# Optimization experiments

Measured on AMD Instinct MI355X. Metric: run time of the kernel, lower is better.

## Reference

```python
import jax, jax.numpy as jnp
import numpy as np

D = 512      # d_model
H = 8        # n_heads
NB = 6       # n_blocks
V = 32000    # vocab
F = 2048     # ff_size
B, L = 2, 1024
EPS = 1e-6
NEG = -1e10  # -INF used by create_causal_bias


def _ln(x, g, b):
    m = jnp.mean(x, axis=-1, keepdims=True)
    v = jnp.mean((x - m) ** 2, axis=-1, keepdims=True)
    return (x - m) * jax.lax.rsqrt(v + EPS) * g + b


def _split_heads(t):
    b, l, _ = t.shape
    return t.reshape(b, l, H, D // H).transpose(0, 2, 1, 3)  # [B,H,L,dh]


def _mha(q_in, kv_in, bias, wq, wk, wv, wo):
    # manual q@k^T / sqrt(dh) + bias -> softmax -> @v -> out proj (no bias terms)
    q = _split_heads(q_in @ wq)
    k = _split_heads(kv_in @ wk)
    v = _split_heads(kv_in @ wv)
    s = jnp.einsum('bhqd,bhkd->bhqk', q, k) / (D // H) ** 0.5 + bias
    a = jax.nn.softmax(s, axis=-1)
    o = jnp.einsum('bhqk,bhkd->bhqd', a, v)
    b_, _, l, _ = o.shape
    o = o.transpose(0, 2, 1, 3).reshape(b_, l, D)
    return o @ wo


def _pos_enc(length):
    pos = jnp.arange(length, dtype=jnp.float32)
    half = D // 2
    i = jnp.arange(half, dtype=jnp.float32)
    scaled = pos[:, None] / jnp.power(10000.0, i / half)[None]
    return jnp.concatenate([jnp.sin(scaled), jnp.cos(scaled)], axis=1)  # [L, D]


def setup_inputs() -> dict:
    key = jax.random.key(0)
    ks = jax.random.split(key, 16)
    s = 0.02
    inp = {
        'x': jax.random.randint(ks[0], (B, L), 0, V, dtype=jnp.int32),
        'ctx': jax.random.normal(ks[1], (B, L, D), jnp.float32),
        'emb': jax.random.normal(ks[2], (V, D), jnp.float32) * s,
        'wq_s': jax.random.normal(ks[3], (NB, D, D), jnp.float32) * s,
        'wk_s': jax.random.normal(ks[4], (NB, D, D), jnp.float32) * s,
        'wv_s': jax.random.normal(ks[5], (NB, D, D), jnp.float32) * s,
        'wo_s': jax.random.normal(ks[6], (NB, D, D), jnp.float32) * s,
        'wq_c': jax.random.normal(ks[7], (NB, D, D), jnp.float32) * s,
        'wk_c': jax.random.normal(ks[8], (NB, D, D), jnp.float32) * s,
        'wv_c': jax.random.normal(ks[9], (NB, D, D), jnp.float32) * s,
        'wo_c': jax.random.normal(ks[10], (NB, D, D), jnp.float32) * s,
        'w1': jax.random.normal(ks[11], (NB, D, F), jnp.float32) * s,
        'b1': jnp.zeros((NB, F), jnp.float32),
        'w2': jax.random.normal(ks[12], (NB, F, D), jnp.float32) * s,
        'b2': jnp.zeros((NB, D), jnp.float32),
        'ln1_g': jnp.ones((NB, D), jnp.float32), 'ln1_b': jnp.zeros((NB, D), jnp.float32),
        'ln2_g': jnp.ones((NB, D), jnp.float32), 'ln2_b': jnp.zeros((NB, D), jnp.float32),
        'ln3_g': jnp.ones((NB, D), jnp.float32), 'ln3_b': jnp.zeros((NB, D), jnp.float32),
        'lnf_g': jnp.ones((D,), jnp.float32), 'lnf_b': jnp.zeros((D,), jnp.float32),
    }
    return inp


def reference(x, ctx, emb, wq_s, wk_s, wv_s, wo_s, wq_c, wk_c, wv_c, wo_c,
              w1, b1, w2, b2, ln1_g, ln1_b, ln2_g, ln2_b, ln3_g, ln3_b,
              lnf_g, lnf_b):
    length = x.shape[1]
    # embedding * sqrt(D) + sinusoidal positional encoding
    h = emb[x] * jnp.sqrt(jnp.float32(D)) + _pos_enc(length)[None]
    # causal bias: upper triangle (excl. diag) filled with -INF, shape [1,1,L,L]
    causal = ((1.0 - jnp.tril(jnp.ones((length, length), jnp.float32))) * NEG)[None, None]
    zero_bias = jnp.zeros((1, 1, 1, 1), jnp.float32)  # no masking of encoder ctx
    for i in range(NB):
        y = _ln(h, ln1_g[i], ln1_b[i])
        h = h + _mha(y, y, causal, wq_s[i], wk_s[i], wv_s[i], wo_s[i])
        y = _ln(h, ln2_g[i], ln2_b[i])
        h = h + _mha(y, ctx, zero_bias, wq_c[i], wk_c[i], wv_c[i], wo_c[i])
        y = _ln(h, ln3_g[i], ln3_b[i])
        h = h + (jax.nn.relu(y @ w1[i] + b1[i]) @ w2[i] + b2[i])
    h = _ln(h, lnf_g, lnf_b)
    # emb2logits: shared embedding projection
    return jnp.einsum('bld,vd->blv', h, emb)
```

## Files before the change

### kernel.cpp

```cpp
#include <hip/hip_runtime.h>
#include <math.h>

#define Bv 2
#define Lv 1024
#define Dv 512
#define Hv 8
#define DH 64
#define Fv 2048
#define NBv 6
#define Vv 32000
#define Mv (Bv*Lv)
#define QS 1536
#define KVS 6144
#define NEGINF -1e10f

typedef __attribute__((ext_vector_type(8))) short short8;
typedef __attribute__((ext_vector_type(4))) short short4v;
typedef __attribute__((ext_vector_type(4))) float floatx4;
typedef __attribute__((address_space(1))) const void gvoid;
typedef __attribute__((address_space(3))) void svoid;

__device__ __forceinline__ short f2bf(float f) {
    union { float f; unsigned u; } v; v.f = f;
    unsigned r = v.u + 0x7fffu + ((v.u >> 16) & 1u);
    return (short)(r >> 16);
}

__global__ __launch_bounds__(256)
void embed_kernel(const int* __restrict__ xi, const float* __restrict__ emb,
                  float* __restrict__ h)
{
    const int row = blockIdx.x;
    const int l   = row & (Lv - 1);
    const int tok = xi[row];
    const int tid = threadIdx.x;
#pragma unroll
    for (int s = 0; s < 2; ++s) {
        const int d  = tid + s * 256;
        const int dd = d & 255;
        const float freq = powf(10000.f, (float)dd * (1.f / 256.f));
        const float arg  = (float)l / freq;
        const float pe   = (d < 256) ? sinf(arg) : cosf(arg);
        h[(size_t)row * Dv + d] = emb[(size_t)tok * Dv + d] * 22.62741699796952f + pe;
    }
}

__global__ __launch_bounds__(256)
void cvt_kernel(const float* __restrict__ X, short* __restrict__ Y)
{
    const int i = (blockIdx.x * 256 + threadIdx.x) * 4;
    const float4 v = *(const float4*)(X + i);
    short4v p; p.x = f2bf(v.x); p.y = f2bf(v.y); p.z = f2bf(v.z); p.w = f2bf(v.w);
    *(short4v*)(Y + i) = p;
}

__global__ __launch_bounds__(256)
void tr_cvt(const float* __restrict__ src, short* __restrict__ dst,
            int K, int N, size_t dstZ, size_t dstOff)
{
    __shared__ float t[64][65];
    const int z  = blockIdx.z;
    const int n0 = blockIdx.x * 64, k0 = blockIdx.y * 64;
    const int tid = threadIdx.x;
    const float* s = src + (size_t)z * K * N;
    short* d = dst + (size_t)z * dstZ + dstOff;

    const int kr = tid >> 2, nc = (tid & 3) * 16;
#pragma unroll
    for (int j = 0; j < 16; j += 4) {
        const float4 v = *(const float4*)(s + (size_t)(k0 + kr) * N + n0 + nc + j);
        t[kr][nc + j + 0] = v.x; t[kr][nc + j + 1] = v.y;
        t[kr][nc + j + 2] = v.z; t[kr][nc + j + 3] = v.w;
    }
    __syncthreads();
    const int nr = tid >> 2, kc = (tid & 3) * 16;
    short8 o0, o1;
#pragma unroll
    for (int j = 0; j < 8; ++j)  o0[j] = f2bf(t[kc + j][nr]);
#pragma unroll
    for (int j = 0; j < 8; ++j)  o1[j] = f2bf(t[kc + 8 + j][nr]);
    *(short8*)(d + (size_t)(n0 + nr) * K + k0 + kc)     = o0;
    *(short8*)(d + (size_t)(n0 + nr) * K + k0 + kc + 8) = o1;
}

__global__ __launch_bounds__(256)
void ln_kernel(const float* __restrict__ X, const float* __restrict__ g,
               const float* __restrict__ bta, short* __restrict__ Y)
{
    const int row = blockIdx.x, tid = threadIdx.x;
    const float* xr = X + (size_t)row * Dv;
    const float x0 = xr[tid], x1 = xr[tid + 256];
    __shared__ float red[4];

    float s = x0 + x1;
#pragma unroll
    for (int off = 32; off; off >>= 1) s += __shfl_xor(s, off);
    if ((tid & 63) == 0) red[tid >> 6] = s;
    __syncthreads();
    const float mean = (red[0] + red[1] + red[2] + red[3]) * (1.f / Dv);
    __syncthreads();

    const float d0 = x0 - mean, d1 = x1 - mean;
    float v = d0 * d0 + d1 * d1;
#pragma unroll
    for (int off = 32; off; off >>= 1) v += __shfl_xor(v, off);
    if ((tid & 63) == 0) red[tid >> 6] = v;
    __syncthreads();
    const float var  = (red[0] + red[1] + red[2] + red[3]) * (1.f / Dv);
    const float rstd = rsqrtf(var + 1e-6f);

    Y[(size_t)row * Dv + tid]       = f2bf(d0 * rstd * g[tid]       + bta[tid]);
    Y[(size_t)row * Dv + tid + 256] = f2bf(d1 * rstd * g[tid + 256] + bta[tid + 256]);
}

template <int BM, int BN, int BK, int BMODE, bool OUTBF, bool SWZ, bool DBUF>
__global__ __launch_bounds__(256)
void mgemm(const short* __restrict__ A, const float* __restrict__ B,
           void* __restrict__ Cp, int M, int N, int K,
           const float* __restrict__ bias,
           const float* __restrict__ residual, int relu)
{
    constexpr int WMT = BM / 2, MI = WMT / 16, NF = BN / 32;
    constexpr int CPR = BK / 8;
    constexpr int NBUF = (DBUF && BMODE == 2) ? 2 : 1;
    __shared__ short As[NBUF * BM * BK];
    __shared__ short Bs[NBUF * BN * BK];
    const int tid  = threadIdx.x;
    const int wave = tid >> 6, lane = tid & 63;
    const int wm = wave & 1, wn = wave >> 1;
    const int quad = lane >> 4, l16 = lane & 15;

    int m0, n0;
    if (SWZ) {
        const int wg = (blockIdx.x & 7) * 500 + (blockIdx.x >> 3);
        m0 = (wg & 15) * BM;
        n0 = (wg >> 4) * BN;
    } else {
        m0 = blockIdx.y * BM;
        n0 = blockIdx.x * BN;
    }

    floatx4 acc[MI][NF];
#pragma unroll
    for (int i = 0; i < MI; ++i)
#pragma unroll
        for (int j = 0; j < NF; ++j)
            acc[i][j] = (floatx4){0.f, 0.f, 0.f, 0.f};

    auto computeTile = [&](const short* Asb, const short* Bsb) {
#pragma unroll
        for (int kk = 0; kk < BK; kk += 32) {
            short8 af[MI];
#pragma unroll
            for (int mi = 0; mi < MI; ++mi) {
                const int r = wm * WMT + mi * 16 + l16;
                af[mi] = *(const short8*)&Asb[r * BK + ((kk + quad * 8) ^ ((r & 7) << 3))];
            }
#pragma unroll
            for (int ni = 0; ni < NF; ++ni) {
                const int n = wn * (BN / 2) + ni * 16 + l16;
                const short8 bfr = *(const short8*)&Bsb[n * BK + ((kk + quad * 8) ^ ((n & 7) << 3))];
#pragma unroll
                for (int mi = 0; mi < MI; ++mi)
                    acc[mi][ni] = __builtin_amdgcn_mfma_f32_16x16x32_bf16(af[mi], bfr, acc[mi][ni], 0, 0, 0);
            }
        }
    };

    if constexpr (DBUF && BMODE == 2) {
        const short* Bb = (const short*)B;
        auto stage = [&](int buf, int kbase) {
#pragma unroll
            for (int s = 0; s < (BM * CPR) / 256; ++s) {
                const int c = s * 256 + tid;
                const int row = c / CPR, kp = (c % CPR) * 8;
                const int kps = kp ^ ((row & 7) << 3);
                const short* gp = A + (size_t)(m0 + row) * K + kbase + kps;
                __builtin_amdgcn_global_load_lds((gvoid*)gp,
                    (svoid*)((char*)As + buf * (BM * BK * 2) + c * 16), 16, 0, 0);
            }
#pragma unroll
            for (int s = 0; s < (BN * CPR) / 256; ++s) {
                const int c = s * 256 + tid;
                const int row = c / CPR, kp = (c % CPR) * 8;
                const int kps = kp ^ ((row & 7) << 3);
                const short* gp = Bb + (size_t)(n0 + row) * K + kbase + kps;
                __builtin_amdgcn_global_load_lds((gvoid*)gp,
                    (svoid*)((char*)Bs + buf * (BN * BK * 2) + c * 16), 16, 0, 0);
            }
        };
        stage(0, 0);
        __syncthreads();
        const int NT = K / BK;
        for (int t = 0; t < NT; ++t) {
            const int cur = t & 1;
            if (t + 1 < NT) stage(cur ^ 1, (t + 1) * BK);
            computeTile(As + cur * BM * BK, Bs + cur * BN * BK);
            __syncthreads();
        }
    } else {
        for (int k0 = 0; k0 < K; k0 += BK) {
            __syncthreads();
#pragma unroll
            for (int s = 0; s < (BM * CPR) / 256; ++s) {
                const int c = s * 256 + tid;
                const int row = c / CPR, kp = (c % CPR) * 8;
                const int kps = kp ^ ((row & 7) << 3);
                const short* gp = A + (size_t)(m0 + row) * K + k0 + kps;
                __builtin_amdgcn_global_load_lds((gvoid*)gp, (svoid*)((char*)As + c * 16),
                                                 16, 0, 0);
            }
            if (BMODE == 0) {
                constexpr int QN = BN / 4;
                constexpr int KSTEP = (256 / QN) * 4;
                const int qn  = tid % QN;
                const int kq0 = (tid / QN) * 4;
#pragma unroll
                for (int p = 0; p < BK / KSTEP; ++p) {
                    const int krow = p * KSTEP + kq0;
                    const float* gp = B + (size_t)(k0 + krow) * N + n0 + qn * 4;
                    const float4 r0 = *(const float4*)(gp);
                    const float4 r1 = *(const float4*)(gp + N);
                    const float4 r2 = *(const float4*)(gp + 2 * (size_t)N);
                    const float4 r3 = *(const float4*)(gp + 3 * (size_t)N);
#pragma unroll
                    for (int e = 0; e < 4; ++e) {
                        const int n = qn * 4 + e;
                        short4v p4;
                        p4.x = f2bf(e == 0 ? r0.x : e == 1 ? r0.y : e == 2 ? r0.z : r0.w);
                        p4.y = f2bf(e == 0 ? r1.x : e == 1 ? r1.y : e == 2 ? r1.z : r1.w);
                        p4.z = f2bf(e == 0 ? r2.x : e == 1 ? r2.y : e == 2 ? r2.z : r2.w);
                        p4.w = f2bf(e == 0 ? r3.x : e == 1 ? r3.y : e == 2 ? r3.z : r3.w);
                        *(short4v*)&Bs[n * BK + (krow ^ ((n & 7) << 3))] = p4;
                    }
                }
            } else if (BMODE == 1) {
#pragma unroll
                for (int f = 0; f < (BN * (BK / 4)) / 256; ++f) {
                    const int gidx = f * 256 + tid;
                    const int n = gidx / (BK / 4), q = (gidx % (BK / 4)) * 4;
                    const float4 r = *(const float4*)(B + (size_t)(n0 + n) * K + k0 + q);
                    short4v p; p.x = f2bf(r.x); p.y = f2bf(r.y); p.z = f2bf(r.z); p.w = f2bf(r.w);
                    *(short4v*)&Bs[n * BK + (q ^ ((n & 7) << 3))] = p;
                }
            } else {
                const short* Bb = (const short*)B;
#pragma unroll
                for (int s = 0; s < (BN * CPR) / 256; ++s) {
                    const int c = s * 256 + tid;
                    const int row = c / CPR, kp = (c % CPR) * 8;
                    const int kps = kp ^ ((row & 7) << 3);
                    const short* gp = Bb + (size_t)(n0 + row) * K + k0 + kps;
                    __builtin_amdgcn_global_load_lds((gvoid*)gp, (svoid*)((char*)Bs + c * 16),
                                                     16, 0, 0);
                }
            }
            __syncthreads();
            computeTile(As, Bs);
        }
    }

#pragma unroll
    for (int mi = 0; mi < MI; ++mi)
#pragma unroll
        for (int ni = 0; ni < NF; ++ni)
#pragma unroll
            for (int r = 0; r < 4; ++r) {
                const int m = m0 + wm * WMT + mi * 16 + quad * 4 + r;
                const int n = n0 + wn * (BN / 2) + ni * 16 + l16;
                float v = acc[mi][ni][r];
                if (bias)     v += bias[n];
                if (residual) v += residual[(size_t)m * N + n];
                if (relu)     v = fmaxf(v, 0.f);
                if (OUTBF) ((short*)Cp)[(size_t)m * N + n] = f2bf(v);
                else       ((float*)Cp)[(size_t)m * N + n] = v;
            }
}

__global__ __launch_bounds__(256)
void qkv_gemm(const short* __restrict__ Aq, const short* __restrict__ Akv,
              const float* __restrict__ B0, const float* __restrict__ B1,
              const float* __restrict__ B2, short* __restrict__ QKV)
{
    constexpr int BM = 64, BN = 64, BK = 64, N = Dv, K = Dv;
    constexpr int WMT = BM / 2, MI = WMT / 16, NF = 2;
    constexpr int CPR = BK / 8;
    __shared__ short As[BM * BK];
    __shared__ short Bs[BN * BK];
    const int tid  = threadIdx.x;
    const int wave = tid >> 6, lane = tid & 63;
    const int wm = wave & 1, wn = wave >> 1;
    const int quad = lane >> 4, l16 = lane & 15;
    const int n0g = blockIdx.x * BN, m0 = blockIdx.y * BM;
    const int wsel = n0g >> 9, n0 = n0g & 511;
    const short* A = (wsel == 0) ? Aq : Akv;
    const float* B = (wsel == 0) ? B0 : (wsel == 1) ? B1 : B2;

    floatx4 acc[MI][NF];
#pragma unroll
    for (int i = 0; i < MI; ++i)
#pragma unroll
        for (int j = 0; j < NF; ++j)
            acc[i][j] = (floatx4){0.f, 0.f, 0.f, 0.f};

    for (int k0 = 0; k0 < K; k0 += BK) {
        __syncthreads();
#pragma unroll
        for (int s = 0; s < (BM * CPR) / 256; ++s) {
            const int c = s * 256 + tid;
            const int row = c / CPR, kp = (c % CPR) * 8;
            const int kps = kp ^ ((row & 7) << 3);
            const short* gp = A + (size_t)(m0 + row) * K + k0 + kps;
            __builtin_amdgcn_global_load_lds((gvoid*)gp, (svoid*)((char*)As + c * 16),
                                             16, 0, 0);
        }
        {
            constexpr int QN = BN / 4;
            const int qn  = tid % QN;
            const int krow = (tid / QN) * 4;
            const float* gp = B + (size_t)(k0 + krow) * N + n0 + qn * 4;
            const float4 r0 = *(const float4*)(gp);
            const float4 r1 = *(const float4*)(gp + N);
            const float4 r2 = *(const float4*)(gp + 2 * (size_t)N);
            const float4 r3 = *(const float4*)(gp + 3 * (size_t)N);
#pragma unroll
            for (int e = 0; e < 4; ++e) {
                const int n = qn * 4 + e;
                short4v p4;
                p4.x = f2bf(e == 0 ? r0.x : e == 1 ? r0.y : e == 2 ? r0.z : r0.w);
                p4.y = f2bf(e == 0 ? r1.x : e == 1 ? r1.y : e == 2 ? r1.z : r1.w);
                p4.z = f2bf(e == 0 ? r2.x : e == 1 ? r2.y : e == 2 ? r2.z : r2.w);
                p4.w = f2bf(e == 0 ? r3.x : e == 1 ? r3.y : e == 2 ? r3.z : r3.w);
                *(short4v*)&Bs[n * BK + (krow ^ ((n & 7) << 3))] = p4;
            }
        }
        __syncthreads();
#pragma unroll
        for (int kk = 0; kk < BK; kk += 32) {
            short8 af[MI];
#pragma unroll
            for (int mi = 0; mi < MI; ++mi) {
                const int r = wm * WMT + mi * 16 + l16;
                af[mi] = *(short8*)&As[r * BK + ((kk + quad * 8) ^ ((r & 7) << 3))];
            }
#pragma unroll
            for (int ni = 0; ni < NF; ++ni) {
                const int n = wn * 32 + ni * 16 + l16;
                const short8 bfr = *(short8*)&Bs[n * BK + ((kk + quad * 8) ^ ((n & 7) << 3))];
#pragma unroll
                for (int mi = 0; mi < MI; ++mi)
                    acc[mi][ni] = __builtin_amdgcn_mfma_f32_16x16x32_bf16(af[mi], bfr, acc[mi][ni], 0, 0, 0);
            }
        }
    }

#pragma unroll
    for (int mi = 0; mi < MI; ++mi)
#pragma unroll
        for (int ni = 0; ni < NF; ++ni)
#pragma unroll
            for (int r = 0; r < 4; ++r) {
                const int m = m0 + wm * WMT + mi * 16 + quad * 4 + r;
                const int n = n0g + wn * 32 + ni * 16 + l16;
                QKV[(size_t)m * QS + n] = f2bf(acc[mi][ni][r]);
            }
}

__global__ __launch_bounds__(256)
void attn_mfma(const short* __restrict__ Qp, int qstr,
               const short* __restrict__ Kp, const short* __restrict__ Vp, int kvstr,
               short* __restrict__ Op, int causal)
{
    constexpr int PK = 72;
    __shared__ short Ks[64 * PK];
    __shared__ short Vs[64 * PK];
    __shared__ short Ps[4][16 * PK];
    const int tid  = threadIdx.x;
    const int wave = tid >> 6, lane = tid & 63;
    const int quad = lane >> 4, l16 = lane & 15;
    const int hh = blockIdx.y, bb = blockIdx.z;
    const int q0 = blockIdx.x * 64;
    const size_t qbase  = (size_t)bb * Lv * qstr  + (size_t)hh * DH;
    const size_t kvbase = (size_t)bb * Lv * kvstr + (size_t)hh * DH;
    const size_t obase  = (size_t)bb * Lv * Dv + (size_t)hh * DH;

    short8 aq[2];
    {
        const short* qp = Qp + qbase + (size_t)(q0 + wave * 16 + l16) * qstr + quad * 8;
        aq[0] = *(const short8*)qp;
        aq[1] = *(const short8*)(qp + 32);
    }

    floatx4 o[4];
#pragma unroll
    for (int i = 0; i < 4; ++i) o[i] = (floatx4){0.f, 0.f, 0.f, 0.f};
    float mrow[4] = {-3.4e38f, -3.4e38f, -3.4e38f, -3.4e38f};
    float srow[4] = {0.f, 0.f, 0.f, 0.f};

    const int ntiles = causal ? (q0 / 64 + 1) : (Lv / 64);

    for (int t = 0; t < ntiles; ++t) {
        const int j0 = t * 64;
        __syncthreads();
#pragma unroll
        for (int s = 0; s < 2; ++s) {
            const int c = s * 256 + tid;
            const int j = c >> 3, off = (c & 7) * 8;
            const size_t grow = kvbase + (size_t)(j0 + j) * kvstr + off;
            *(short8*)&Ks[j * PK + off] = *(const short8*)(Kp + grow);
            const short8 v = *(const short8*)(Vp + grow);
            const int jx = j ^ ((c & 7) << 3);
#pragma unroll
            for (int e = 0; e < 8; ++e)
                Vs[(off + e) * PK + jx] = v[e];
        }
        __syncthreads();

        floatx4 sf[4];
#pragma unroll
        for (int nf = 0; nf < 4; ++nf) {
            const short8 bk0 = *(const short8*)&Ks[(nf * 16 + l16) * PK + quad * 8];
            const short8 bk1 = *(const short8*)&Ks[(nf * 16 + l16) * PK + 32 + quad * 8];
            floatx4 z = (floatx4){0.f, 0.f, 0.f, 0.f};
            z = __builtin_amdgcn_mfma_f32_16x16x32_bf16(aq[0], bk0, z, 0, 0, 0);
            z = __builtin_amdgcn_mfma_f32_16x16x32_bf16(aq[1], bk1, z, 0, 0, 0);
            sf[nf] = z;
        }

        const bool mask = causal && (j0 == q0);
#pragma unroll
        for (int nf = 0; nf < 4; ++nf) {
            const int jabs = j0 + nf * 16 + l16;
#pragma unroll
            for (int r = 0; r < 4; ++r) {
                float v = sf[nf][r] * 0.125f;
                if (mask && jabs > q0 + wave * 16 + quad * 4 + r) v = NEGINF;
                sf[nf][r] = v;
            }
        }

#pragma unroll
        for (int r = 0; r < 4; ++r) {
            float v = fmaxf(fmaxf(sf[0][r], sf[1][r]), fmaxf(sf[2][r], sf[3][r]));
            v = fmaxf(v, __shfl_xor(v, 1));
            v = fmaxf(v, __shfl_xor(v, 2));
            v = fmaxf(v, __shfl_xor(v, 4));
            v = fmaxf(v, __shfl_xor(v, 8));
            const float mnew = fmaxf(mrow[r], v);
            const float corr = __expf(mrow[r] - mnew);
            mrow[r] = mnew;
            srow[r] *= corr;
#pragma unroll
            for (int nf = 0; nf < 4; ++nf) o[nf][r] *= corr;
        }

#pragma unroll
        for (int nf = 0; nf < 4; ++nf) {
#pragma unroll
            for (int r = 0; r < 4; ++r) {
                const float pv = __expf(sf[nf][r] - mrow[r]);
                srow[r] += pv;
                Ps[wave][(quad * 4 + r) * PK + nf * 16 + l16] = f2bf(pv);
            }
        }
        __builtin_amdgcn_wave_barrier();

        const short8 pa0 = *(const short8*)&Ps[wave][l16 * PK + quad * 8];
        const short8 pa1 = *(const short8*)&Ps[wave][l16 * PK + 32 + quad * 8];
#pragma unroll
        for (int nf = 0; nf < 4; ++nf) {
            const int d   = nf * 16 + l16;
            const int swz = ((d >> 3) & 7) << 3;
            const short8 bv0 = *(const short8*)&Vs[d * PK + ((quad * 8) ^ swz)];
            const short8 bv1 = *(const short8*)&Vs[d * PK + ((32 + quad * 8) ^ swz)];
            o[nf] = __builtin_amdgcn_mfma_f32_16x16x32_bf16(pa0, bv0, o[nf], 0, 0, 0);
            o[nf] = __builtin_amdgcn_mfma_f32_16x16x32_bf16(pa1, bv1, o[nf], 0, 0, 0);
        }
    }

#pragma unroll
    for (int r = 0; r < 4; ++r) {
        float s = srow[r];
        s += __shfl_xor(s, 1);
        s += __shfl_xor(s, 2);
        s += __shfl_xor(s, 4);
        s += __shfl_xor(s, 8);
        srow[r] = 1.f / s;
    }
#pragma unroll
    for (int nf = 0; nf < 4; ++nf)
#pragma unroll
        for (int r = 0; r < 4; ++r) {
            const size_t addr = obase + (size_t)(q0 + wave * 16 + quad * 4 + r) * Dv
                              + nf * 16 + l16;
            Op[addr] = f2bf(o[nf][r] * srow[r]);
        }
}

extern "C" void kernel_launch(void* const* d_in, const int* in_sizes, int n_in,
                              void* d_out, int out_size, void* d_ws, size_t ws_size,
                              hipStream_t stream)
{
    const int*   x    = (const int*)  d_in[0];
    const float* ctx  = (const float*)d_in[1];
    const float* emb  = (const float*)d_in[2];
    const float* wq_s = (const float*)d_in[3];
    const float* wk_s = (const float*)d_in[4];
    const float* wv_s = (const float*)d_in[5];
    const float* wo_s = (const float*)d_in[6];
    const float* wq_c = (const float*)d_in[7];
    const float* wk_c = (const float*)d_in[8];
    const float* wv_c = (const float*)d_in[9];
    const float* wo_c = (const float*)d_in[10];
    const float* w1   = (const float*)d_in[11];
    const float* b1   = (const float*)d_in[12];
    const float* w2   = (const float*)d_in[13];
    const float* b2   = (const float*)d_in[14];
    const float* ln1g = (const float*)d_in[15];
    const float* ln1b = (const float*)d_in[16];
    const float* ln2g = (const float*)d_in[17];
    const float* ln2b = (const float*)d_in[18];
    const float* ln3g = (const float*)d_in[19];
    const float* ln3b = (const float*)d_in[20];
    const float* lnfg = (const float*)d_in[21];
    const float* lnfb = (const float*)d_in[22];
    float* out = (float*)d_out;

    char* wsb = (char*)d_ws;
    const dim3 blk(256);
    const dim3 gAttn(Lv / 64, Hv, Bv);
    const dim3 gV(16 * 250);

    if (ws_size >= (150u << 20)) {
        float* h      = (float*)(wsb);
        short* y_bf   = (short*)(wsb + (4u   << 20));
        short* ao_bf  = (short*)(wsb + (6u   << 20));
        short* ctx_bf = (short*)(wsb + (8u   << 20));
        short* qkv    = (short*)(wsb + (10u  << 20));
        short* ff_bf  = (short*)(wsb + (16u  << 20));
        short* qb     = (short*)(wsb + (24u  << 20));
        short* kvc    = (short*)(wsb + (26u  << 20));
        short* wqkv_s = (short*)(wsb + (50u  << 20));
        short* wo_s_t = (short*)(wsb + (60u  << 20));
        short* wq_c_t = (short*)(wsb + (64u  << 20));
        short* wo_c_t = (short*)(wsb + (68u  << 20));
        short* kvw    = (short*)(wsb + (72u  << 20));
        short* w1t    = (short*)(wsb + (79u  << 20));
        short* w2t    = (short*)(wsb + (92u  << 20));
        short* emb_bf = (short*)(wsb + (105u << 20));

        embed_kernel<<<Mv, blk, 0, stream>>>(x, emb, h);
        cvt_kernel<<<(Mv * Dv) / 1024, blk, 0, stream>>>(ctx, ctx_bf);
        cvt_kernel<<<(Vv * Dv) / 1024, blk, 0, stream>>>(emb, emb_bf);

        const dim3 gT55(8, 8, NBv);
        const dim3 gT5F(Fv / 64, 8, NBv);
        const dim3 gTF5(8, Fv / 64, NBv);
        tr_cvt<<<gT55, blk, 0, stream>>>(wq_s, wqkv_s, Dv, Dv, (size_t)QS * Dv, 0);
        tr_cvt<<<gT55, blk, 0, stream>>>(wk_s, wqkv_s, Dv, Dv, (size_t)QS * Dv, (size_t)Dv * Dv);
        tr_cvt<<<gT55, blk, 0, stream>>>(wv_s, wqkv_s, Dv, Dv, (size_t)QS * Dv, (size_t)2 * Dv * Dv);
        tr_cvt<<<gT55, blk, 0, stream>>>(wo_s, wo_s_t, Dv, Dv, (size_t)Dv * Dv, 0);
        tr_cvt<<<gT55, blk, 0, stream>>>(wq_c, wq_c_t, Dv, Dv, (size_t)Dv * Dv, 0);
        tr_cvt<<<gT55, blk, 0, stream>>>(wo_c, wo_c_t, Dv, Dv, (size_t)Dv * Dv, 0);
        tr_cvt<<<gT55, blk, 0, stream>>>(wk_c, kvw, Dv, Dv, (size_t)2 * Dv * Dv, 0);
        tr_cvt<<<gT55, blk, 0, stream>>>(wv_c, kvw, Dv, Dv, (size_t)2 * Dv * Dv, (size_t)Dv * Dv);
        tr_cvt<<<gT5F, blk, 0, stream>>>(w1, w1t, Dv, Fv, (size_t)Fv * Dv, 0);
        tr_cvt<<<gTF5, blk, 0, stream>>>(w2, w2t, Fv, Dv, (size_t)Dv * Fv, 0);

        {
            const dim3 g(KVS / 64, Mv / 128);
            mgemm<128, 64, 64, 2, true, false, true><<<g, blk, 0, stream>>>(
                ctx_bf, (const float*)kvw, kvc, Mv, KVS, Dv, nullptr, nullptr, 0);
        }

        const dim3 gQKV(QS / 64, Mv / 64);
        const dim3 gD(Dv / 64, Mv / 32);
        const dim3 gF1(Fv / 128, Mv / 64);

        for (int i = 0; i < NBv; ++i) {
            ln_kernel<<<Mv, blk, 0, stream>>>(h, ln1g + i * Dv, ln1b + i * Dv, y_bf);
            mgemm<64, 64, 64, 2, true, false, true><<<gQKV, blk, 0, stream>>>(
                y_bf, (const float*)(wqkv_s + (size_t)i * QS * Dv), qkv,
                Mv, QS, Dv, nullptr, nullptr, 0);
            attn_mfma<<<gAttn, blk, 0, stream>>>(qkv, QS, qkv + 512, qkv + 1024, QS, ao_bf, 1);
            mgemm<32, 64, 64, 2, false, false, true><<<gD, blk, 0, stream>>>(
                ao_bf, (const float*)(wo_s_t + (size_t)i * Dv * Dv), h,
                Mv, Dv, Dv, nullptr, h, 0);
            ln_kernel<<<Mv, blk, 0, stream>>>(h, ln2g + i * Dv, ln2b + i * Dv, y_bf);
            mgemm<32, 64, 64, 2, true, false, true><<<gD, blk, 0, stream>>>(
                y_bf, (const float*)(wq_c_t + (size_t)i * Dv * Dv), qb,
                Mv, Dv, Dv, nullptr, nullptr, 0);
            attn_mfma<<<gAttn, blk, 0, stream>>>(qb, Dv,
                kvc + (size_t)i * 1024, kvc + (size_t)i * 1024 + 512, KVS, ao_bf, 0);
            mgemm<32, 64, 64, 2, false, false, true><<<gD, blk, 0, stream>>>(
                ao_bf, (const float*)(wo_c_t + (size_t)i * Dv * Dv), h,
                Mv, Dv, Dv, nullptr, h, 0);
            ln_kernel<<<Mv, blk, 0, stream>>>(h, ln3g + i * Dv, ln3b + i * Dv, y_bf);
            mgemm<64, 128, 64, 2, true, false, true><<<gF1, blk, 0, stream>>>(
                y_bf, (const float*)(w1t + (size_t)i * Fv * Dv), ff_bf,
                Mv, Fv, Dv, b1 + (size_t)i * Fv, nullptr, 1);
            mgemm<32, 64, 64, 2, false, false, true><<<gD, blk, 0, stream>>>(
                ff_bf, (const float*)(w2t + (size_t)i * Dv * Fv), h,
                Mv, Dv, Fv, b2 + (size_t)i * Dv, h, 0);
        }

        ln_kernel<<<Mv, blk, 0, stream>>>(h, lnfg, lnfb, y_bf);
        mgemm<128, 128, 64, 2, false, true, false><<<gV, blk, 0, stream>>>(
            y_bf, (const float*)emb_bf, out, Mv, Vv, Dv, nullptr, nullptr, 0);
    } else {
        float* h      = (float*)(wsb);
        short* y_bf   = (short*)(wsb + (4u  << 20));
        short* ao_bf  = (short*)(wsb + (6u  << 20));
        short* ctx_bf = (short*)(wsb + (8u  << 20));
        short* qkv    = (short*)(wsb + (10u << 20));
        short* ff_bf  = (short*)(wsb + (10u << 20));
        short* emb_bf = (short*)(wsb + (18u << 20));
        const bool fastv = ws_size >= (52u << 20);

        const dim3 gQKV(QS / 64, Mv / 64);
        const dim3 gD(Dv / 64, Mv / 32);
        const dim3 gF(Fv / 128, Mv / 64);

        embed_kernel<<<Mv, blk, 0, stream>>>(x, emb, h);
        cvt_kernel<<<(Mv * Dv) / 1024, blk, 0, stream>>>(ctx, ctx_bf);
        if (fastv)
            cvt_kernel<<<(Vv * Dv) / 1024, blk, 0, stream>>>(emb, emb_bf);

        for (int i = 0; i < NBv; ++i) {
            const size_t wOff = (size_t)i * Dv * Dv;
            ln_kernel<<<Mv, blk, 0, stream>>>(h, ln1g + i * Dv, ln1b + i * Dv, y_bf);
            qkv_gemm<<<gQKV, blk, 0, stream>>>(y_bf, y_bf,
                                               wq_s + wOff, wk_s + wOff, wv_s + wOff, qkv);
            attn_mfma<<<gAttn, blk, 0, stream>>>(qkv, QS, qkv + 512, qkv + 1024, QS, ao_bf, 1);
            mgemm<32, 64, 64, 0, false, false, false><<<gD, blk, 0, stream>>>(
                ao_bf, wo_s + wOff, h, Mv, Dv, Dv, nullptr, h, 0);
            ln_kernel<<<Mv, blk, 0, stream>>>(h, ln2g + i * Dv, ln2b + i * Dv, y_bf);
            qkv_gemm<<<gQKV, blk, 0, stream>>>(y_bf, ctx_bf,
                                               wq_c + wOff, wk_c + wOff, wv_c + wOff, qkv);
            attn_mfma<<<gAttn, blk, 0, stream>>>(qkv, QS, qkv + 512, qkv + 1024, QS, ao_bf, 0);
            mgemm<32, 64, 64, 0, false, false, false><<<gD, blk, 0, stream>>>(
                ao_bf, wo_c + wOff, h, Mv, Dv, Dv, nullptr, h, 0);
            ln_kernel<<<Mv, blk, 0, stream>>>(h, ln3g + i * Dv, ln3b + i * Dv, y_bf);
            mgemm<64, 128, 64, 0, true, false, false><<<gF, blk, 0, stream>>>(
                y_bf, w1 + (size_t)i * Dv * Fv, ff_bf, Mv, Fv, Dv,
                b1 + (size_t)i * Fv, nullptr, 1);
            mgemm<32, 64, 64, 0, false, false, false><<<gD, blk, 0, stream>>>(
                ff_bf, w2 + (size_t)i * Fv * Dv, h, Mv, Dv, Fv,
                b2 + (size_t)i * Dv, h, 0);
        }

        ln_kernel<<<Mv, blk, 0, stream>>>(h, lnfg, lnfb, y_bf);
        if (fastv)
            mgemm<128, 128, 64, 2, false, true, false><<<gV, blk, 0, stream>>>(
                y_bf, (const float*)emb_bf, out, Mv, Vv, Dv, nullptr, nullptr, 0);
        else
            mgemm<128, 128, 64, 1, false, true, false><<<gV, blk, 0, stream>>>(
                y_bf, emb, out, Mv, Vv, Dv, nullptr, nullptr, 0);
    }
}
```

Before: 1.407 ms.

## Fuse layernorm into following GEMMs and double-buffer the vocab projection

Adds an lngemm kernel that loads a 32-row fp32 tile of h, computes layernorm statistics in-block, writes normalized bf16 rows into LDS, then runs an MFMA GEMM over the full K=512 with double-buffered B tiles. It replaces the ln_kernel plus GEMM pairs for QKV, cross-attn Q and FF1, removing the y_bf round trip and three launches per block. Each tile recomputes the layernorm for its rows, so the work is repeated across N-tiles. Smaller M-tiles also change occupancy. The final vocab GEMM is switched to double buffering.

```diff
diff --git a/kernel.cpp b/kernel.cpp
--- a/kernel.cpp
+++ b/kernel.cpp
@@ -111,6 +111,124 @@
 
     Y[(size_t)row * Dv + tid]       = f2bf(d0 * rstd * g[tid]       + bta[tid]);
     Y[(size_t)row * Dv + tid + 256] = f2bf(d1 * rstd * g[tid + 256] + bta[tid + 256]);
+}
+
+template <int BN>
+__global__ __launch_bounds__(256)
+void lngemm(const float* __restrict__ h, const float* __restrict__ g,
+            const float* __restrict__ bta, const short* __restrict__ Bb,
+            short* __restrict__ Cp, int N,
+            const float* __restrict__ bias, int relu)
+{
+    constexpr int BM = 32, BK = 64, K = 512;
+    constexpr int WMT = BM / 2, MI = WMT / 16, NF = BN / 32;
+    constexpr int CPR = BK / 8;
+    __shared__ short As[BM * K];
+    __shared__ short Bs[2 * BN * BK];
+    const int tid  = threadIdx.x;
+    const int wave = tid >> 6, lane = tid & 63;
+    const int wm = wave & 1, wn = wave >> 1;
+    const int quad = lane >> 4, l16 = lane & 15;
+    const int m0 = blockIdx.y * BM, n0 = blockIdx.x * BN;
+
+    {
+        const int r  = tid >> 3;
+        const int c0 = (tid & 7) * 64;
+        const float* hr = h + (size_t)(m0 + r) * K + c0;
+        float s1 = 0.f, s2 = 0.f;
+#pragma unroll
+        for (int j = 0; j < 64; j += 4) {
+            const float4 v = *(const float4*)(hr + j);
+            s1 += v.x + v.y + v.z + v.w;
+            s2 += v.x * v.x + v.y * v.y + v.z * v.z + v.w * v.w;
+        }
+#pragma unroll
+        for (int off = 4; off; off >>= 1) {
+            s1 += __shfl_xor(s1, off);
+            s2 += __shfl_xor(s2, off);
+        }
+        const float mean = s1 * (1.f / 512.f);
+        const float rstd = rsqrtf(s2 * (1.f / 512.f) - mean * mean + 1e-6f);
+#pragma unroll
+        for (int j8 = 0; j8 < 8; ++j8) {
+            const float4 a0 = *(const float4*)(hr + j8 * 8);
+            const float4 a1 = *(const float4*)(hr + j8 * 8 + 4);
+            const float4 g0 = *(const float4*)(g + c0 + j8 * 8);
+            const float4 g1 = *(const float4*)(g + c0 + j8 * 8 + 4);
+            const float4 t0 = *(const float4*)(bta + c0 + j8 * 8);
+            const float4 t1 = *(const float4*)(bta + c0 + j8 * 8 + 4);
+            short8 o;
+            o[0] = f2bf((a0.x - mean) * rstd * g0.x + t0.x);
+            o[1] = f2bf((a0.y - mean) * rstd * g0.y + t0.y);
+            o[2] = f2bf((a0.z - mean) * rstd * g0.z + t0.z);
+            o[3] = f2bf((a0.w - mean) * rstd * g0.w + t0.w);
+            o[4] = f2bf((a1.x - mean) * rstd * g1.x + t1.x);
+            o[5] = f2bf((a1.y - mean) * rstd * g1.y + t1.y);
+            o[6] = f2bf((a1.z - mean) * rstd * g1.z + t1.z);
+            o[7] = f2bf((a1.w - mean) * rstd * g1.w + t1.w);
+            const int kc = c0 + j8 * 8;
+            *(short8*)&As[r * K + (kc ^ ((r & 7) << 3))] = o;
+        }
+    }
+
+    auto stageB = [&](int buf, int kbase) {
+#pragma unroll
+        for (int s = 0; s < (BN * CPR) / 256; ++s) {
+            const int c = s * 256 + tid;
+            const int row = c / CPR, kp = (c % CPR) * 8;
+            const int kps = kp ^ ((row & 7) << 3);
+            const short* gp = Bb + (size_t)(n0 + row) * K + kbase + kps;
+            __builtin_amdgcn_global_load_lds((gvoid*)gp,
+                (svoid*)((char*)Bs + buf * (BN * BK * 2) + c * 16), 16, 0, 0);
+        }
+    };
+
+    floatx4 acc[MI][NF];
+#pragma unroll
+    for (int i = 0; i < MI; ++i)
+#pragma unroll
+        for (int j = 0; j < NF; ++j)
+            acc[i][j] = (floatx4){0.f, 0.f, 0.f, 0.f};
+
+    stageB(0, 0);
+    __syncthreads();
+    constexpr int NT = K / BK;
+    for (int t = 0; t < NT; ++t) {
+        const int cur = t & 1;
+        if (t + 1 < NT) stageB(cur ^ 1, (t + 1) * BK);
+#pragma unroll
+        for (int kk = 0; kk < BK; kk += 32) {
+            short8 af[MI];
+#pragma unroll
+            for (int mi = 0; mi < MI; ++mi) {
+                const int r = wm * WMT + mi * 16 + l16;
+                af[mi] = *(const short8*)&As[r * K + ((t * BK + kk + quad * 8) ^ ((r & 7) << 3))];
+            }
+#pragma unroll
+            for (int ni = 0; ni < NF; ++ni) {
+                const int n = wn * (BN / 2) + ni * 16 + l16;
+                const short8 bfr = *(const short8*)&Bs[cur * BN * BK + n * BK + ((kk + quad * 8) ^ ((n & 7) << 3))];
+#pragma unroll
+                for (int mi = 0; mi < MI; ++mi)
+                    acc[mi][ni] = __builtin_amdgcn_mfma_f32_16x16x32_bf16(af[mi], bfr, acc[mi][ni], 0, 0, 0);
+            }
+        }
+        __syncthreads();
+    }
+
+#pragma unroll
+    for (int mi = 0; mi < MI; ++mi)
+#pragma unroll
+        for (int ni = 0; ni < NF; ++ni)
+#pragma unroll
+            for (int r = 0; r < 4; ++r) {
+                const int m = m0 + wm * WMT + mi * 16 + quad * 4 + r;
+                const int n = n0 + wn * (BN / 2) + ni * 16 + l16;
+                float v = acc[mi][ni][r];
+                if (bias) v += bias[n];
+                if (relu) v = fmaxf(v, 0.f);
+                Cp[(size_t)m * N + n] = f2bf(v);
+            }
 }
 
 template <int BM, int BN, int BK, int BMODE, bool OUTBF, bool SWZ, bool DBUF>
@@ -573,39 +691,35 @@
                 ctx_bf, (const float*)kvw, kvc, Mv, KVS, Dv, nullptr, nullptr, 0);
         }
 
-        const dim3 gQKV(QS / 64, Mv / 64);
+        const dim3 gQKV(QS / 64, Mv / 32);
+        const dim3 gQ(Dv / 64, Mv / 32);
+        const dim3 gFF1(Fv / 64, Mv / 32);
         const dim3 gD(Dv / 64, Mv / 32);
         const dim3 gF1(Fv / 128, Mv / 64);
 
         for (int i = 0; i < NBv; ++i) {
-            ln_kernel<<<Mv, blk, 0, stream>>>(h, ln1g + i * Dv, ln1b + i * Dv, y_bf);
-            mgemm<64, 64, 64, 2, true, false, true><<<gQKV, blk, 0, stream>>>(
-                y_bf, (const float*)(wqkv_s + (size_t)i * QS * Dv), qkv,
-                Mv, QS, Dv, nullptr, nullptr, 0);
+            lngemm<64><<<gQKV, blk, 0, stream>>>(h, ln1g + i * Dv, ln1b + i * Dv,
+                wqkv_s + (size_t)i * QS * Dv, qkv, QS, nullptr, 0);
             attn_mfma<<<gAttn, blk, 0, stream>>>(qkv, QS, qkv + 512, qkv + 1024, QS, ao_bf, 1);
             mgemm<32, 64, 64, 2, false, false, true><<<gD, blk, 0, stream>>>(
                 ao_bf, (const float*)(wo_s_t + (size_t)i * Dv * Dv), h,
                 Mv, Dv, Dv, nullptr, h, 0);
-            ln_kernel<<<Mv, blk, 0, stream>>>(h, ln2g + i * Dv, ln2b + i * Dv, y_bf);
-            mgemm<32, 64, 64, 2, true, false, true><<<gD, blk, 0, stream>>>(
-                y_bf, (const float*)(wq_c_t + (size_t)i * Dv * Dv), qb,
-                Mv, Dv, Dv, nullptr, nullptr, 0);
+            lngemm<64><<<gQ, blk, 0, stream>>>(h, ln2g + i * Dv, ln2b + i * Dv,
+                wq_c_t + (size_t)i * Dv * Dv, qb, Dv, nullptr, 0);
             attn_mfma<<<gAttn, blk, 0, stream>>>(qb, Dv,
                 kvc + (size_t)i * 1024, kvc + (size_t)i * 1024 + 512, KVS, ao_bf, 0);
             mgemm<32, 64, 64, 2, false, false, true><<<gD, blk, 0, stream>>>(
                 ao_bf, (const float*)(wo_c_t + (size_t)i * Dv * Dv), h,
                 Mv, Dv, Dv, nullptr, h, 0);
-            ln_kernel<<<Mv, blk, 0, stream>>>(h, ln3g + i * Dv, ln3b + i * Dv, y_bf);
-            mgemm<64, 128, 64, 2, true, false, true><<<gF1, blk, 0, stream>>>(
-                y_bf, (const float*)(w1t + (size_t)i * Fv * Dv), ff_bf,
-                Mv, Fv, Dv, b1 + (size_t)i * Fv, nullptr, 1);
+            lngemm<64><<<gFF1, blk, 0, stream>>>(h, ln3g + i * Dv, ln3b + i * Dv,
+                w1t + (size_t)i * Fv * Dv, ff_bf, Fv, b1 + (size_t)i * Fv, 1);
             mgemm<32, 64, 64, 2, false, false, true><<<gD, blk, 0, stream>>>(
                 ff_bf, (const float*)(w2t + (size_t)i * Dv * Fv), h,
                 Mv, Dv, Fv, b2 + (size_t)i * Dv, h, 0);
         }
 
         ln_kernel<<<Mv, blk, 0, stream>>>(h, lnfg, lnfb, y_bf);
-        mgemm<128, 128, 64, 2, false, true, false><<<gV, blk, 0, stream>>>(
+        mgemm<128, 128, 64, 2, false, true, true><<<gV, blk, 0, stream>>>(
             y_bf, (const float*)emb_bf, out, Mv, Vv, Dv, nullptr, nullptr, 0);
     } else {
         float* h      = (float*)(wsb);
```

Measured after the change: 2.245 ms. 59.6% more time.
